# Kernel tuning notes

Hardware: AMD Instinct MI355X
Metric: run time of the kernel (lower is better)

## Reference

```python
import jax, jax.numpy as jnp
import numpy as np

N, E, F, HID, PC, HEADS = 100000, 1600000, 128, 128, 16, 4
RATIO = 0.8
NEG_SLOPE = 0.2
BIG_NEG = -1e9


def setup_inputs() -> dict:
    ks = jax.random.split(jax.random.key(0), 20)
    def g(k, shape, fan):
        return jax.random.normal(k, shape, jnp.float32) / np.float32(np.sqrt(fan))
    return {
        "x": jax.random.normal(ks[0], (N, F), jnp.float32),
        "edge_index": jax.random.randint(ks[1], (2, E), 0, N, dtype=jnp.int32),
        "edge_attr": jax.random.uniform(ks[2], (E, 1), dtype=jnp.float32),
        "W1": g(ks[3], (F, PC), F),
        "att_src1": g(ks[4], (HEADS, PC // HEADS), PC // HEADS),
        "att_dst1": g(ks[5], (HEADS, PC // HEADS), PC // HEADS),
        "We1": g(ks[6], (1, PC), 1),
        "att_edge1": g(ks[7], (HEADS, PC // HEADS), PC // HEADS),
        "b1": jnp.zeros((PC,), jnp.float32),
        "Wrel": g(ks[8], (PC, 1), PC),
        "brel": jnp.zeros((1,), jnp.float32),
        "Wroot": g(ks[9], (PC, 1), PC),
        "W2": g(ks[10], (PC, HID), PC),
        "att_src2": g(ks[11], (1, HID), HID),
        "att_dst2": g(ks[12], (1, HID), HID),
        "We2": g(ks[13], (1, HID), 1),
        "att_edge2": g(ks[14], (1, HID), HID),
        "b2": jnp.zeros((HID,), jnp.float32),
        "Wg": g(ks[15], (HID, 1), HID),
        "bg": jnp.zeros((1,), jnp.float32),
    }


def gat_conv(h_in, src, dst, e_attr, W, a_s, a_d, We, a_e, b, num_nodes, mask=None):
    """PyG GATConv (add_self_loops=False, eval-mode so dropout is identity)."""
    H, D = a_s.shape
    h = (h_in @ W).reshape(-1, H, D)                      # [N,H,D]
    al_s = jnp.einsum('nhd,hd->nh', h, a_s)               # alpha contribution of source
    al_d = jnp.einsum('nhd,hd->nh', h, a_d)               # alpha contribution of dest
    he = (e_attr @ We).reshape(-1, H, D)                  # [E,H,D] edge features
    al_e = jnp.einsum('ehd,hd->eh', he, a_e)              # [E,H]
    logits = jax.nn.leaky_relu(al_s[src] + al_d[dst] + al_e, NEG_SLOPE)  # [E,H]
    if mask is not None:
        logits = jnp.where(mask[:, None], logits, BIG_NEG)
    # segment softmax over incoming edges of each destination node
    m = jnp.maximum(jax.ops.segment_max(logits, dst, num_segments=num_nodes), BIG_NEG)
    num = jnp.exp(logits - m[dst])
    if mask is not None:
        num = jnp.where(mask[:, None], num, 0.0)
    den = jax.ops.segment_sum(num, dst, num_segments=num_nodes)
    coef = num / jnp.maximum(den[dst], 1e-16)             # [E,H]
    out = jax.ops.segment_sum(coef[:, :, None] * h[src], dst, num_segments=num_nodes)
    return out.reshape(num_nodes, H * D) + b


def _forward(x, edge_attr, W1, att_src1, att_dst1, We1, att_edge1, b1,
             Wrel, brel, Wroot, W2, att_src2, att_dst2, We2, att_edge2, b2,
             Wg, bg, edge_index):
    n = x.shape[0]
    src, dst = edge_index[0], edge_index[1]
    h1 = jax.nn.relu(gat_conv(x, src, dst, edge_attr, W1, att_src1, att_dst1, We1, att_edge1, b1, n))
    # --- SAGPooling: GraphConv score -> tanh -> top-k -> masked subgraph (n > node_threshold always) ---
    agg = jax.ops.segment_sum(h1[src], dst, num_segments=n)           # neighbor sum
    score = (agg @ Wrel + brel + h1 @ Wroot).reshape(-1)              # GraphConv(16 -> 1)
    k = int(np.ceil(RATIO * n))                                       # static
    vals, perm = jax.lax.top_k(score, k)
    new_idx = jnp.full((n,), -1, dtype=jnp.int32).at[perm].set(jnp.arange(k, dtype=jnp.int32))
    src_n, dst_n = new_idx[src], new_idx[dst]
    emask = (src_n >= 0) & (dst_n >= 0)                               # edges with both ends kept
    src2 = jnp.where(emask, src_n, 0)
    dst2 = jnp.where(emask, dst_n, 0)
    x2 = h1[perm] * jnp.tanh(vals)[:, None]                           # gate kept nodes
    h2 = jax.nn.relu(gat_conv(x2, src2, dst2, edge_attr, W2, att_src2, att_dst2, We2, att_edge2, b2, k, mask=emask))
    # --- AttentionalAggregation + MaxAggregation over the single graph (index = zeros) ---
    gate = jax.nn.softmax(h2 @ Wg + bg, axis=0)                       # [k,1]
    att = (gate * h2).sum(axis=0, keepdims=True)                      # [1,HID]
    mx = h2.max(axis=0, keepdims=True)                                # [1,HID]
    return jnp.concatenate([att, mx], axis=1)                         # [1,2*HID]


def reference(x, edge_index, edge_attr, W1, att_src1, att_dst1, We1, att_edge1, b1,
              Wrel, brel, Wroot, W2, att_src2, att_dst2, We2, att_edge2, b2, Wg, bg):
    return _forward(x, edge_attr, W1, att_src1, att_dst1, We1, att_edge1, b1,
                    Wrel, brel, Wroot, W2, att_src2, att_dst2, We2, att_edge2, b2,
                    Wg, bg, edge_index)
```

## Files before the change

### kernel.cpp

```cpp
#include <hip/hip_runtime.h>
#include <hip/hip_bf16.h>

#define Nn 100000
#define Ee 1600000
#define Kk 80000
#define NB ((Nn + 255) / 256)
#define NBK 196
#define CHK 8192
#define G2B 2048

typedef unsigned int uint;
typedef unsigned short ushort;

struct Scal {
    uint prefix, remaining, needEq;
    float c1[4];
    float c2;
    uint gmaxOrd;
    float deng;
    float attnum[128];
    uint mxOrd[128];
};

__device__ __forceinline__ uint f2ord(float f) {
    uint b = __float_as_uint(f);
    return (b & 0x80000000u) ? ~b : (b | 0x80000000u);
}
__device__ __forceinline__ float ord2f(uint u) {
    uint b = (u & 0x80000000u) ? (u ^ 0x80000000u) : ~u;
    return __uint_as_float(b);
}
__device__ __forceinline__ float lrelu(float v) { return v > 0.f ? v : 0.2f * v; }
__device__ __forceinline__ float2 bf2f2(uint u) {
    return make_float2(__uint_as_float(u << 16), __uint_as_float(u & 0xFFFF0000u));
}
__device__ __forceinline__ uint f2bf2(float a, float b) {
    __hip_bfloat162 h;
    h.x = __float2bfloat16(a);
    h.y = __float2bfloat16(b);
    return *(uint*)&h;
}

__global__ __launch_bounds__(256) void initK(uint* bcnt, uint* hist, Scal* sc) {
    int i = blockIdx.x * 256 + threadIdx.x;
    if (i < NBK) bcnt[i] = 0u;
    if (i < 256) hist[i] = 0u;
    if (i < 128) { sc->attnum[i] = 0.f; sc->mxOrd[i] = f2ord(0.0f); }
    if (i == 0) {
        sc->prefix = 0u; sc->remaining = Kk; sc->needEq = 0u;
        sc->deng = 0.f; sc->gmaxOrd = f2ord(-1e30f);
    }
}

__global__ void constK(const float* We1, const float* ae1, const float* We2, const float* ae2,
                       Scal* sc) {
    if (threadIdx.x == 0) {
        for (int h = 0; h < 4; h++) {
            float s = 0.f;
            for (int d = 0; d < 4; d++) s += We1[h * 4 + d] * ae1[h * 4 + d];
            sc->c1[h] = s;
        }
        float s2 = 0.f;
        for (int d = 0; d < 128; d++) s2 += We2[d] * ae2[d];
        sc->c2 = s2;
    }
}

__global__ __launch_bounds__(256) void nodeL1(const float* __restrict__ x,
                                              const float* __restrict__ W1,
                                              const float* __restrict__ as1,
                                              const float* __restrict__ ad1,
                                              float* __restrict__ hpre,
                                              float* __restrict__ alS1,
                                              float* __restrict__ alD1) {
    __shared__ float Ws[128 * 16];
    __shared__ float s_as[16], s_ad[16];
    for (int i = threadIdx.x; i < 2048; i += 256) Ws[i] = W1[i];
    if (threadIdx.x < 16) { s_as[threadIdx.x] = as1[threadIdx.x]; s_ad[threadIdx.x] = ad1[threadIdx.x]; }
    __syncthreads();
    int n = blockIdx.x * 256 + threadIdx.x;
    if (n >= Nn) return;
    float acc[16];
#pragma unroll
    for (int j = 0; j < 16; j++) acc[j] = 0.f;
    const float4* xr = (const float4*)(x + (size_t)n * 128);
    for (int t4 = 0; t4 < 32; t4++) {
        float4 xv = xr[t4];
#pragma unroll
        for (int j = 0; j < 16; j++) {
            acc[j] += xv.x * Ws[(t4 * 4 + 0) * 16 + j];
            acc[j] += xv.y * Ws[(t4 * 4 + 1) * 16 + j];
            acc[j] += xv.z * Ws[(t4 * 4 + 2) * 16 + j];
            acc[j] += xv.w * Ws[(t4 * 4 + 3) * 16 + j];
        }
    }
    float* hp = hpre + (size_t)n * 16;
#pragma unroll
    for (int j = 0; j < 16; j++) hp[j] = acc[j];
#pragma unroll
    for (int h = 0; h < 4; h++) {
        float s = 0.f, d = 0.f;
#pragma unroll
        for (int q = 0; q < 4; q++) {
            s += acc[h * 4 + q] * s_as[h * 4 + q];
            d += acc[h * 4 + q] * s_ad[h * 4 + q];
        }
        alS1[n * 4 + h] = s;
        alD1[n * 4 + h] = d;
    }
}

__global__ __launch_bounds__(256) void bucketCnt(const int* __restrict__ ei, uint* __restrict__ bcnt) {
    __shared__ uint h[NBK];
    if (threadIdx.x < NBK) h[threadIdx.x] = 0u;
    __syncthreads();
    for (int e = blockIdx.x * 256 + threadIdx.x; e < Ee; e += gridDim.x * 256)
        atomicAdd(&h[((uint)ei[Ee + e]) >> 9], 1u);
    __syncthreads();
    if (threadIdx.x < NBK && h[threadIdx.x]) atomicAdd(&bcnt[threadIdx.x], h[threadIdx.x]);
}

__global__ __launch_bounds__(256) void scanBk(const uint* __restrict__ bcnt, uint* __restrict__ boff,
                                              uint* __restrict__ gcur) {
    __shared__ uint s[256];
    int t = threadIdx.x;
    uint v = (t < NBK) ? bcnt[t] : 0u;
    s[t] = v;
    __syncthreads();
    for (int off = 1; off < 256; off <<= 1) {
        uint u = (t >= off) ? s[t - off] : 0u;
        __syncthreads();
        s[t] += u;
        __syncthreads();
    }
    if (t < NBK) { boff[t] = s[t] - v; gcur[t] = 0u; }
    if (t == 0) boff[NBK] = Ee;
}

__global__ __launch_bounds__(256) void binScat(const int* __restrict__ ei, const float* __restrict__ ea,
                                               const uint* __restrict__ boff, uint* __restrict__ gcur,
                                               uint2* __restrict__ bsE, ushort* __restrict__ bsD) {
    __shared__ uint h[NBK], base[NBK], h2[NBK];
    int t = threadIdx.x;
    if (t < NBK) h[t] = 0u;
    __syncthreads();
    int estart = blockIdx.x * CHK;
    int eend = min(Ee, estart + CHK);
    for (int e = estart + t; e < eend; e += 256)
        atomicAdd(&h[((uint)ei[Ee + e]) >> 9], 1u);
    __syncthreads();
    if (t < NBK) { base[t] = atomicAdd(&gcur[t], h[t]); h2[t] = 0u; }
    __syncthreads();
    for (int e = estart + t; e < eend; e += 256) {
        uint d = (uint)ei[Ee + e];
        uint b = d >> 9;
        uint r = atomicAdd(&h2[b], 1u);
        uint pos = boff[b] + base[b] + r;
        bsE[pos] = make_uint2((uint)ei[e], __float_as_uint(ea[e]));
        bsD[pos] = (ushort)(d & 511u);
    }
}

__global__ __launch_bounds__(256) void rankK(const uint* __restrict__ boff, const ushort* __restrict__ bsD,
                                             ushort* __restrict__ bsR, uint* __restrict__ deg) {
    __shared__ uint ldeg[512];
    int b = blockIdx.x, t = threadIdx.x;
    ldeg[t] = 0u; ldeg[t + 256] = 0u;
    __syncthreads();
    uint r0 = boff[b], r1 = boff[b + 1];
    for (uint i = r0 + t; i < r1; i += 256)
        bsR[i] = (ushort)atomicAdd(&ldeg[bsD[i]], 1u);
    __syncthreads();
    int nd = b * 512 + t;
    if (nd < Nn) deg[nd] = ldeg[t];
    nd = b * 512 + 256 + t;
    if (nd < Nn) deg[nd] = ldeg[256 + t];
}

__global__ __launch_bounds__(256) void scanA(const uint* __restrict__ deg, uint* __restrict__ rowstart,
                                             uint* __restrict__ blkSum) {
    __shared__ uint s[256];
    int i = blockIdx.x * 256 + threadIdx.x;
    uint v = (i < Nn) ? deg[i] : 0u;
    s[threadIdx.x] = v;
    __syncthreads();
    for (int off = 1; off < 256; off <<= 1) {
        uint t = (threadIdx.x >= off) ? s[threadIdx.x - off] : 0u;
        __syncthreads();
        s[threadIdx.x] += t;
        __syncthreads();
    }
    if (i < Nn) rowstart[i] = s[threadIdx.x] - v;
    if (threadIdx.x == 255) blkSum[blockIdx.x] = s[255];
}

__global__ __launch_bounds__(512) void scanB(const uint* __restrict__ blkSum, uint* __restrict__ blkOff) {
    __shared__ uint s[512];
    uint v = (threadIdx.x < NB) ? blkSum[threadIdx.x] : 0u;
    s[threadIdx.x] = v;
    __syncthreads();
    for (int off = 1; off < 512; off <<= 1) {
        uint t = (threadIdx.x >= off) ? s[threadIdx.x - off] : 0u;
        __syncthreads();
        s[threadIdx.x] += t;
        __syncthreads();
    }
    if (threadIdx.x < NB) blkOff[threadIdx.x] = s[threadIdx.x] - v;
}

__global__ __launch_bounds__(256) void scanC(uint* __restrict__ rowstart, const uint* __restrict__ blkOff) {
    int i = blockIdx.x * 256 + threadIdx.x;
    if (i < Nn) rowstart[i] += blkOff[blockIdx.x];
    if (i == 0) rowstart[Nn] = Ee;
}

__global__ __launch_bounds__(256) void placeK(const uint* __restrict__ boff, const uint2* __restrict__ bsE,
                                              const ushort* __restrict__ bsD, const ushort* __restrict__ bsR,
                                              const uint* __restrict__ rowstart, uint2* __restrict__ csr_p8) {
    __shared__ uint srs[512];
    int b = blockIdx.x, t = threadIdx.x;
    int nd = b * 512 + t;
    srs[t] = (nd < Nn) ? rowstart[nd] : 0u;
    nd = b * 512 + 256 + t;
    srs[256 + t] = (nd < Nn) ? rowstart[nd] : 0u;
    __syncthreads();
    uint r0 = boff[b], r1 = boff[b + 1];
    for (uint i = r0 + t; i < r1; i += 256)
        csr_p8[srs[bsD[i]] + bsR[i]] = bsE[i];
}

__global__ __launch_bounds__(256) void edgeP1(const uint2* __restrict__ csr_p8,
                                              const float* __restrict__ alS1,
                                              const Scal* __restrict__ scc,
                                              float4* __restrict__ csr_p1, int* __restrict__ csr_src) {
    int i = blockIdx.x * 256 + threadIdx.x;
    if (i >= Ee) return;
    uint2 p8 = csr_p8[i];
    int s = (int)p8.x;
    float eav = __uint_as_float(p8.y);
    float4 as = *(const float4*)(alS1 + (size_t)s * 4);
    float4 o;
    o.x = as.x + eav * scc->c1[0];
    o.y = as.y + eav * scc->c1[1];
    o.z = as.z + eav * scc->c1[2];
    o.w = as.w + eav * scc->c1[3];
    csr_p1[i] = o;
    csr_src[i] = s;
}

__global__ __launch_bounds__(256) void gather1e(const int* __restrict__ csr_src, const float* __restrict__ csr_p1,
                                                const uint* __restrict__ rowstart, const float* __restrict__ alD1,
                                                const float* __restrict__ hpre,
                                                const float* __restrict__ b1, const float* __restrict__ Wrel,
                                                const float* __restrict__ Wroot,
                                                float* __restrict__ h1, float* __restrict__ p,
                                                float* __restrict__ q) {
    int tid = blockIdx.x * 256 + threadIdx.x;
    if (tid >= Nn * 4) return;
    int d = tid >> 2, h = tid & 3;
    uint r0 = rowstart[d], r1 = rowstart[d + 1];
    float ad = alD1[tid];
    float den = 0.f;
    float4 acc = {0.f, 0.f, 0.f, 0.f};
#pragma unroll 8
    for (uint i = r0; i < r1; i++) {
        float e = __expf(lrelu(csr_p1[(size_t)i * 4 + h] + ad));
        float4 hv = *(const float4*)(hpre + (size_t)csr_src[i] * 16 + h * 4);
        den += e;
        acc.x += e * hv.x; acc.y += e * hv.y;
        acc.z += e * hv.z; acc.w += e * hv.w;
    }
    float inv = 1.f / fmaxf(den, 1e-16f);
    float4 o;
    o.x = fmaxf(acc.x * inv + b1[h * 4 + 0], 0.f);
    o.y = fmaxf(acc.y * inv + b1[h * 4 + 1], 0.f);
    o.z = fmaxf(acc.z * inv + b1[h * 4 + 2], 0.f);
    o.w = fmaxf(acc.w * inv + b1[h * 4 + 3], 0.f);
    *(float4*)(h1 + (size_t)d * 16 + h * 4) = o;
    float pp = o.x * Wrel[h * 4 + 0] + o.y * Wrel[h * 4 + 1] + o.z * Wrel[h * 4 + 2] + o.w * Wrel[h * 4 + 3];
    float qq = o.x * Wroot[h * 4 + 0] + o.y * Wroot[h * 4 + 1] + o.z * Wroot[h * 4 + 2] + o.w * Wroot[h * 4 + 3];
    pp += __shfl_xor(pp, 1); pp += __shfl_xor(pp, 2);
    qq += __shfl_xor(qq, 1); qq += __shfl_xor(qq, 2);
    if (h == 0) { p[d] = pp; q[d] = qq; }
}

__global__ __launch_bounds__(256) void scoreK2(const int* __restrict__ csr_src, const uint* __restrict__ rowstart,
                                               const float* __restrict__ p, const float* __restrict__ q,
                                               const float* __restrict__ brel,
                                               float* __restrict__ score, uint* __restrict__ dkey) {
    int d = blockIdx.x * 256 + threadIdx.x;
    if (d >= Nn) return;
    uint r0 = rowstart[d], r1 = rowstart[d + 1];
    float s = brel[0] + q[d];
#pragma unroll 8
    for (uint i = r0; i < r1; i++) s += p[csr_src[i]];
    score[d] = s;
    dkey[d] = ~f2ord(s);
}

__global__ __launch_bounds__(256) void histK(const uint* __restrict__ dkey, const Scal* __restrict__ sc,
                                             uint* __restrict__ hist, int shift) {
    __shared__ uint lh[256];
    lh[threadIdx.x] = 0u;
    __syncthreads();
    int i = blockIdx.x * 256 + threadIdx.x;
    if (i < Nn) {
        uint d = dkey[i];
        bool ok = (shift == 24) || ((d >> (shift + 8)) == sc->prefix);
        if (ok) atomicAdd(&lh[(d >> shift) & 255u], 1u);
    }
    __syncthreads();
    if (lh[threadIdx.x]) atomicAdd(&hist[threadIdx.x], lh[threadIdx.x]);
}

__global__ __launch_bounds__(256) void selP(Scal* sc, uint* hist) {
    __shared__ uint s[256];
    int t = threadIdx.x;
    uint c = hist[t];
    s[t] = c;
    __syncthreads();
    for (int off = 1; off < 256; off <<= 1) {
        uint v = (t >= off) ? s[t - off] : 0u;
        __syncthreads();
        s[t] += v;
        __syncthreads();
    }
    uint rem = sc->remaining;
    uint cum = s[t];
    uint cumex = cum - c;
    if (cum >= rem && cumex < rem) {
        sc->remaining = rem - cumex;
        sc->prefix = (sc->prefix << 8) | (uint)t;
    }
    hist[t] = 0u;
}

__global__ __launch_bounds__(256) void cntK(const uint* __restrict__ dkey, const Scal* __restrict__ sc,
                                            uint* __restrict__ blkLt, uint* __restrict__ blkEq) {
    int i = blockIdx.x * 256 + threadIdx.x;
    uint ut = sc->prefix;
    bool lt = (i < Nn) && (dkey[i] < ut);
    bool eq = (i < Nn) && (dkey[i] == ut);
    __shared__ uint sl[4], se[4];
    unsigned long long bl = __ballot(lt), be = __ballot(eq);
    int lane = threadIdx.x & 63, w = threadIdx.x >> 6;
    if (lane == 0) { sl[w] = (uint)__popcll(bl); se[w] = (uint)__popcll(be); }
    __syncthreads();
    if (threadIdx.x == 0) {
        blkLt[blockIdx.x] = sl[0] + sl[1] + sl[2] + sl[3];
        blkEq[blockIdx.x] = se[0] + se[1] + se[2] + se[3];
    }
}

__global__ __launch_bounds__(512) void prefP(Scal* sc, const uint* __restrict__ blkLt,
                                             const uint* __restrict__ blkEq, uint* __restrict__ eqPref) {
    __shared__ uint se[512];
    __shared__ uint sl[512];
    int t = threadIdx.x;
    uint e = (t < NB) ? blkEq[t] : 0u;
    uint l = (t < NB) ? blkLt[t] : 0u;
    se[t] = e; sl[t] = l;
    __syncthreads();
    for (int off = 1; off < 512; off <<= 1) {
        uint v1 = (t >= off) ? se[t - off] : 0u;
        uint v2 = (t >= off) ? sl[t - off] : 0u;
        __syncthreads();
        se[t] += v1; sl[t] += v2;
        __syncthreads();
    }
    if (t < NB) eqPref[t] = se[t] - e;
    if (t == 511) sc->needEq = Kk - sl[511];
}

__global__ __launch_bounds__(256) void keptK(const uint* __restrict__ dkey, const Scal* __restrict__ sc,
                                             const uint* __restrict__ eqPref, int* __restrict__ kept) {
    int i = blockIdx.x * 256 + threadIdx.x;
    uint ut = sc->prefix, needEq = sc->needEq;
    bool inr = i < Nn;
    uint d = inr ? dkey[i] : 0xFFFFFFFFu;
    bool isLt = inr && (d < ut);
    bool isEq = inr && (d == ut);
    __shared__ uint wcnt[4];
    unsigned long long mask = __ballot(isEq);
    int lane = threadIdx.x & 63, w = threadIdx.x >> 6;
    uint lanePre = (uint)__popcll(mask & ((1ull << lane) - 1ull));
    if (lane == 0) wcnt[w] = (uint)__popcll(mask);
    __syncthreads();
    uint wo = 0;
    for (int q = 0; q < 4; q++) if (q < w) wo += wcnt[q];
    uint rank = eqPref[blockIdx.x] + wo + lanePre;
    if (inr) kept[i] = (isLt || (isEq && rank < needEq)) ? 1 : 0;
}

__global__ __launch_bounds__(256) void nodeL2(const float* __restrict__ h1, const float* __restrict__ score,
                                              const int* __restrict__ kept, const float* __restrict__ W2,
                                              const float* __restrict__ as2, const float* __restrict__ ad2,
                                              __hip_bfloat162* __restrict__ h2b, float* __restrict__ alS2,
                                              float* __restrict__ alD2) {
    __shared__ float Ws[16 * 128];
    for (int i = threadIdx.x; i < 2048; i += 256) Ws[i] = W2[i];
    __syncthreads();
    int wid = (blockIdx.x * 256 + threadIdx.x) >> 6;
    int lane = threadIdx.x & 63;
    if (wid >= Nn) return;
    int n = wid;
    if (!kept[n]) return;
    float t = tanhf(score[n]);
    float x2[16];
    const float* hr = h1 + (size_t)n * 16;
#pragma unroll
    for (int j = 0; j < 16; j++) x2[j] = hr[j] * t;
    int d0 = 2 * lane, d1 = 2 * lane + 1;
    float a0 = 0.f, a1 = 0.f;
    const float2* Wv = (const float2*)Ws;
#pragma unroll
    for (int j = 0; j < 16; j++) {
        float2 wv = Wv[j * 64 + lane];
        a0 += x2[j] * wv.x;
        a1 += x2[j] * wv.y;
    }
    __hip_bfloat162 hb;
    hb.x = __float2bfloat16(a0);
    hb.y = __float2bfloat16(a1);
    h2b[(size_t)n * 64 + lane] = hb;
    float s = a0 * as2[d0] + a1 * as2[d1];
    float dd = a0 * ad2[d0] + a1 * ad2[d1];
#pragma unroll
    for (int off = 32; off; off >>= 1) { s += __shfl_xor(s, off); dd += __shfl_xor(dd, off); }
    if (lane == 0) { alS2[n] = s; alD2[n] = dd; }
}

__global__ __launch_bounds__(256) void edgeP2(const uint2* __restrict__ csr_p8, const int* __restrict__ kept,
                                              const float* __restrict__ alS2,
                                              const Scal* __restrict__ scc, float* __restrict__ csr_p2) {
    int i = blockIdx.x * 256 + threadIdx.x;
    if (i >= Ee) return;
    uint2 p8 = csr_p8[i];
    int s = (int)p8.x;
    float eav = __uint_as_float(p8.y);
    csr_p2[i] = kept[s] ? (alS2[s] + eav * scc->c2) : -1e30f;
}

__global__ __launch_bounds__(256) void gather2f(const int* __restrict__ csr_src,
                                                const float* __restrict__ csr_p2,
                                                const uint* __restrict__ rowstart, const int* __restrict__ kept,
                                                const float* __restrict__ alD2,
                                                const __hip_bfloat162* __restrict__ h2b, const float* __restrict__ b2,
                                                const float* __restrict__ Wg, const float* __restrict__ bg,
                                                float* __restrict__ pacc, float* __restrict__ pmx,
                                                float* __restrict__ pden) {
    __shared__ float sAtt[4][16][8];
    __shared__ float sMx[4][16][8];
    __shared__ float sDen[4];
    int w = threadIdx.x >> 6, lane = threadIdx.x & 63;
    int g = lane >> 4, t = lane & 15;
    float4 b2a = ((const float4*)b2)[t * 2], b2b = ((const float4*)b2)[t * 2 + 1];
    float4 wga = ((const float4*)Wg)[t * 2], wgb = ((const float4*)Wg)[t * 2 + 1];
    float bg0 = bg[0];
    const uint* h2u = (const uint*)h2b;
    float att[8], mx8[8], denP = 0.f;
#pragma unroll
    for (int j = 0; j < 8; j++) { att[j] = 0.f; mx8[j] = 0.f; }
    for (int n = blockIdx.x * 4 + w; n < Nn; n += G2B * 4) {
        if (!kept[n]) continue;
        float ad = alD2[n];
        uint r0 = rowstart[n];
        uint len = rowstart[n + 1] - r0;
        float den = 0.f;
        float acc[8];
#pragma unroll
        for (int d = 0; d < 8; d++) acc[d] = 0.f;
#pragma unroll 2
        for (uint base = 0; base < len; base += 4) {
            uint off = base + (uint)g;
            bool act = off < len;
            uint sidx = act ? (r0 + off) : (r0 + len - 1);
            float pv = act ? csr_p2[sidx] : -1e30f;
            float c = __expf(lrelu(pv + ad));
            int s = csr_src[sidx];
            uint4 hv = *(const uint4*)(h2u + (size_t)s * 64 + t * 4);
            den += c;
            float2 f;
            f = bf2f2(hv.x); acc[0] += c * f.x; acc[1] += c * f.y;
            f = bf2f2(hv.y); acc[2] += c * f.x; acc[3] += c * f.y;
            f = bf2f2(hv.z); acc[4] += c * f.x; acc[5] += c * f.y;
            f = bf2f2(hv.w); acc[6] += c * f.x; acc[7] += c * f.y;
        }
#pragma unroll
        for (int d = 0; d < 8; d++) {
            acc[d] += __shfl_xor(acc[d], 16);
            acc[d] += __shfl_xor(acc[d], 32);
        }
        den += __shfl_xor(den, 16);
        den += __shfl_xor(den, 32);
        float inv = 1.f / fmaxf(den, 1e-16f);
        float o[8];
        o[0] = fmaxf(acc[0] * inv + b2a.x, 0.f);
        o[1] = fmaxf(acc[1] * inv + b2a.y, 0.f);
        o[2] = fmaxf(acc[2] * inv + b2a.z, 0.f);
        o[3] = fmaxf(acc[3] * inv + b2a.w, 0.f);
        o[4] = fmaxf(acc[4] * inv + b2b.x, 0.f);
        o[5] = fmaxf(acc[5] * inv + b2b.y, 0.f);
        o[6] = fmaxf(acc[6] * inv + b2b.z, 0.f);
        o[7] = fmaxf(acc[7] * inv + b2b.w, 0.f);
        float gp = o[0] * wga.x + o[1] * wga.y + o[2] * wga.z + o[3] * wga.w +
                   o[4] * wgb.x + o[5] * wgb.y + o[6] * wgb.z + o[7] * wgb.w;
#pragma unroll
        for (int off = 8; off; off >>= 1) gp += __shfl_xor(gp, off);
        float e = __expf(gp + bg0);
        denP += e;
#pragma unroll
        for (int j = 0; j < 8; j++) {
            att[j] += e * o[j];
            mx8[j] = fmaxf(mx8[j], o[j]);
        }
    }
    if (g == 0) {
#pragma unroll
        for (int j = 0; j < 8; j++) { sAtt[w][t][j] = att[j]; sMx[w][t][j] = mx8[j]; }
    }
    if (lane == 0) sDen[w] = denP;
    __syncthreads();
    int tid = threadIdx.x;
    if (tid < 128) {
        int tt = tid >> 3, j = tid & 7;
        float a = sAtt[0][tt][j] + sAtt[1][tt][j] + sAtt[2][tt][j] + sAtt[3][tt][j];
        float m = fmaxf(fmaxf(sMx[0][tt][j], sMx[1][tt][j]), fmaxf(sMx[2][tt][j], sMx[3][tt][j]));
        pacc[(size_t)blockIdx.x * 128 + tid] = a;
        pmx[(size_t)blockIdx.x * 128 + tid] = m;
    }
    if (tid == 0) pden[blockIdx.x] = sDen[0] + sDen[1] + sDen[2] + sDen[3];
}

__global__ __launch_bounds__(256) void gateRed(const float* __restrict__ pacc, const float* __restrict__ pmx,
                                               const float* __restrict__ pden, Scal* sc) {
    __shared__ float r[256];
    int b = blockIdx.x, tid = threadIdx.x;
    if (b < 128) {
        float a = 0.f, m = 0.f;
        for (int i = tid; i < G2B; i += 256) {
            a += pacc[(size_t)i * 128 + b];
            m = fmaxf(m, pmx[(size_t)i * 128 + b]);
        }
        r[tid] = a;
        __syncthreads();
        for (int off = 128; off; off >>= 1) {
            if (tid < off) r[tid] += r[tid + off];
            __syncthreads();
        }
        float asum = r[0];
        __syncthreads();
        r[tid] = m;
        __syncthreads();
        for (int off = 128; off; off >>= 1) {
            if (tid < off) r[tid] = fmaxf(r[tid], r[tid + off]);
            __syncthreads();
        }
        if (tid == 0) { sc->attnum[b] = asum; sc->mxOrd[b] = f2ord(r[0]); }
    } else {
        float d = 0.f;
        for (int i = tid; i < G2B; i += 256) d += pden[i];
        r[tid] = d;
        __syncthreads();
        for (int off = 128; off; off >>= 1) {
            if (tid < off) r[tid] += r[tid + off];
            __syncthreads();
        }
        if (tid == 0) sc->deng = r[0];
    }
}

__global__ void outK(const Scal* sc, float* out) {
    int d = threadIdx.x;
    if (d < 128) {
        out[d] = sc->attnum[d] / sc->deng;
        out[128 + d] = ord2f(sc->mxOrd[d]);
    }
}

extern "C" void kernel_launch(void* const* d_in, const int* in_sizes, int n_in,
                              void* d_out, int out_size, void* d_ws, size_t ws_size,
                              hipStream_t stream) {
    const float* x = (const float*)d_in[0];
    const int* ei = (const int*)d_in[1];
    const float* ea = (const float*)d_in[2];
    const float* W1 = (const float*)d_in[3];
    const float* as1 = (const float*)d_in[4];
    const float* ad1 = (const float*)d_in[5];
    const float* We1 = (const float*)d_in[6];
    const float* ae1 = (const float*)d_in[7];
    const float* b1 = (const float*)d_in[8];
    const float* Wrel = (const float*)d_in[9];
    const float* brel = (const float*)d_in[10];
    const float* Wroot = (const float*)d_in[11];
    const float* W2 = (const float*)d_in[12];
    const float* as2 = (const float*)d_in[13];
    const float* ad2 = (const float*)d_in[14];
    const float* We2 = (const float*)d_in[15];
    const float* ae2 = (const float*)d_in[16];
    const float* b2 = (const float*)d_in[17];
    const float* Wg = (const float*)d_in[18];
    const float* bg = (const float*)d_in[19];
    float* out = (float*)d_out;

    float* base = (float*)d_ws;
    size_t o = 0;
    auto alloc = [&](size_t nf) { float* p2 = base + o; o += nf; return p2; };
    float4* csr_p1 = (float4*)alloc((size_t)Ee * 4);
    uint2* bsE = (uint2*)csr_p1;
    ushort* bsD = (ushort*)((float*)csr_p1 + (size_t)Ee * 2);
    ushort* bsR = (ushort*)((float*)csr_p1 + (size_t)Ee * 2 + Ee / 2);
    uint2* csr_p8 = (uint2*)alloc((size_t)Ee * 2);
    __hip_bfloat162* h2b = (__hip_bfloat162*)alloc((size_t)Nn * 64);
    float* hpre = alloc((size_t)Nn * 16);
    float* h1 = alloc((size_t)Nn * 16);
    int* csr_src = (int*)alloc(Ee);
    float* csr_p2 = alloc(Ee);
    float* pacc = alloc((size_t)G2B * 128);
    float* pmx = alloc((size_t)G2B * 128);
    float* pden = alloc(G2B);
    float* alS1 = alloc((size_t)Nn * 4);
    float* alD1 = alloc((size_t)Nn * 4);
    float* p = alloc(Nn);
    float* q = alloc(Nn);
    float* score = alloc(Nn);
    uint* dkey = (uint*)alloc(Nn);
    uint* deg = (uint*)alloc(Nn);
    int* kept = (int*)alloc(Nn);
    float* alS2 = alloc(Nn);
    float* alD2 = alloc(Nn);
    uint* rowstart = (uint*)alloc(Nn + 1);
    uint* hist = (uint*)alloc(256);
    uint* blkSum = (uint*)alloc(NB);
    uint* blkOff = (uint*)alloc(NB);
    uint* blkLt = (uint*)alloc(NB);
    uint* blkEq = (uint*)alloc(NB);
    uint* eqPref = (uint*)alloc(NB);
    uint* bcnt = (uint*)alloc(NBK);
    uint* boff = (uint*)alloc(NBK + 1);
    uint* gcur = (uint*)alloc(NBK);
    Scal* sc = (Scal*)alloc(512);

    auto cdiv = [](long a, long b) { return (int)((a + b - 1) / b); };

    initK<<<NB, 256, 0, stream>>>(bcnt, hist, sc);
    constK<<<1, 64, 0, stream>>>(We1, ae1, We2, ae2, sc);
    nodeL1<<<NB, 256, 0, stream>>>(x, W1, as1, ad1, hpre, alS1, alD1);
    bucketCnt<<<512, 256, 0, stream>>>(ei, bcnt);
    scanBk<<<1, 256, 0, stream>>>(bcnt, boff, gcur);
    binScat<<<cdiv(Ee, CHK), 256, 0, stream>>>(ei, ea, boff, gcur, bsE, bsD);
    rankK<<<NBK, 256, 0, stream>>>(boff, bsD, bsR, deg);
    scanA<<<NB, 256, 0, stream>>>(deg, rowstart, blkSum);
    scanB<<<1, 512, 0, stream>>>(blkSum, blkOff);
    scanC<<<NB, 256, 0, stream>>>(rowstart, blkOff);
    placeK<<<NBK, 256, 0, stream>>>(boff, bsE, bsD, bsR, rowstart, csr_p8);
    edgeP1<<<cdiv(Ee, 256), 256, 0, stream>>>(csr_p8, alS1, sc, csr_p1, csr_src);
    gather1e<<<cdiv((long)Nn * 4, 256), 256, 0, stream>>>(csr_src, (const float*)csr_p1, rowstart, alD1,
                                                          hpre, b1, Wrel, Wroot, h1, p, q);
    scoreK2<<<NB, 256, 0, stream>>>(csr_src, rowstart, p, q, brel, score, dkey);
    for (int shift = 24; shift >= 0; shift -= 8) {
        histK<<<NB, 256, 0, stream>>>(dkey, sc, hist, shift);
        selP<<<1, 256, 0, stream>>>(sc, hist);
    }
    cntK<<<NB, 256, 0, stream>>>(dkey, sc, blkLt, blkEq);
    prefP<<<1, 512, 0, stream>>>(sc, blkLt, blkEq, eqPref);
    keptK<<<NB, 256, 0, stream>>>(dkey, sc, eqPref, kept);
    nodeL2<<<cdiv(Nn, 4), 256, 0, stream>>>(h1, score, kept, W2, as2, ad2, h2b, alS2, alD2);
    edgeP2<<<cdiv(Ee, 256), 256, 0, stream>>>(csr_p8, kept, alS2, sc, csr_p2);
    gather2f<<<G2B, 256, 0, stream>>>(csr_src, csr_p2, rowstart, kept, alD2,
                                      h2b, b2, Wg, bg, pacc, pmx, pden);
    gateRed<<<129, 256, 0, stream>>>(pacc, pmx, pden, sc);
    outK<<<1, 128, 0, stream>>>(sc, out);
}
```

Before: 376.2 us.

## Fuse per-edge precompute kernels into gathers and fold constK into initK

Drops the edgeP1 and edgeP2 passes that built per-edge logit arrays (csr_p1, csr_p2, csr_src). The gather kernels now read the packed (src, edge_attr) CSR entry directly and compute the source logit plus edge term on the fly. For layer 2 this uses a per-node alS2k array that nodeL2 sets to -1e30 for dropped nodes. Constant computation is merged into initK, which saves launches and several full-edge write/read passes, at the cost of extra random gathers of alS1/alS2k inside the gather loops.

Result: faster. 342.5 us (-9.0%).

```diff
diff --git a/kernel.cpp b/kernel.cpp
--- a/kernel.cpp
+++ b/kernel.cpp
@@ -34,14 +34,10 @@
 __device__ __forceinline__ float2 bf2f2(uint u) {
     return make_float2(__uint_as_float(u << 16), __uint_as_float(u & 0xFFFF0000u));
 }
-__device__ __forceinline__ uint f2bf2(float a, float b) {
-    __hip_bfloat162 h;
-    h.x = __float2bfloat16(a);
-    h.y = __float2bfloat16(b);
-    return *(uint*)&h;
-}
-
-__global__ __launch_bounds__(256) void initK(uint* bcnt, uint* hist, Scal* sc) {
+
+__global__ __launch_bounds__(256) void initK(uint* bcnt, uint* hist, Scal* sc,
+                                             const float* We1, const float* ae1,
+                                             const float* We2, const float* ae2) {
     int i = blockIdx.x * 256 + threadIdx.x;
     if (i < NBK) bcnt[i] = 0u;
     if (i < 256) hist[i] = 0u;
@@ -49,12 +45,6 @@
     if (i == 0) {
         sc->prefix = 0u; sc->remaining = Kk; sc->needEq = 0u;
         sc->deng = 0.f; sc->gmaxOrd = f2ord(-1e30f);
-    }
-}
-
-__global__ void constK(const float* We1, const float* ae1, const float* We2, const float* ae2,
-                       Scal* sc) {
-    if (threadIdx.x == 0) {
         for (int h = 0; h < 4; h++) {
             float s = 0.f;
             for (int d = 0; d < 4; d++) s += We1[h * 4 + d] * ae1[h * 4 + d];
@@ -229,28 +219,10 @@
         csr_p8[srs[bsD[i]] + bsR[i]] = bsE[i];
 }
 
-__global__ __launch_bounds__(256) void edgeP1(const uint2* __restrict__ csr_p8,
-                                              const float* __restrict__ alS1,
-                                              const Scal* __restrict__ scc,
-                                              float4* __restrict__ csr_p1, int* __restrict__ csr_src) {
-    int i = blockIdx.x * 256 + threadIdx.x;
-    if (i >= Ee) return;
-    uint2 p8 = csr_p8[i];
-    int s = (int)p8.x;
-    float eav = __uint_as_float(p8.y);
-    float4 as = *(const float4*)(alS1 + (size_t)s * 4);
-    float4 o;
-    o.x = as.x + eav * scc->c1[0];
-    o.y = as.y + eav * scc->c1[1];
-    o.z = as.z + eav * scc->c1[2];
-    o.w = as.w + eav * scc->c1[3];
-    csr_p1[i] = o;
-    csr_src[i] = s;
-}
-
-__global__ __launch_bounds__(256) void gather1e(const int* __restrict__ csr_src, const float* __restrict__ csr_p1,
-                                                const uint* __restrict__ rowstart, const float* __restrict__ alD1,
-                                                const float* __restrict__ hpre,
+__global__ __launch_bounds__(256) void gather1f(const uint2* __restrict__ csr_p8,
+                                                const uint* __restrict__ rowstart,
+                                                const float* __restrict__ alS1, const float* __restrict__ alD1,
+                                                const float* __restrict__ hpre, const Scal* __restrict__ scc,
                                                 const float* __restrict__ b1, const float* __restrict__ Wrel,
                                                 const float* __restrict__ Wroot,
                                                 float* __restrict__ h1, float* __restrict__ p,
@@ -260,12 +232,15 @@
     int d = tid >> 2, h = tid & 3;
     uint r0 = rowstart[d], r1 = rowstart[d + 1];
     float ad = alD1[tid];
+    float c1h = scc->c1[h];
     float den = 0.f;
     float4 acc = {0.f, 0.f, 0.f, 0.f};
 #pragma unroll 8
     for (uint i = r0; i < r1; i++) {
-        float e = __expf(lrelu(csr_p1[(size_t)i * 4 + h] + ad));
-        float4 hv = *(const float4*)(hpre + (size_t)csr_src[i] * 16 + h * 4);
+        uint2 p8 = csr_p8[i];
+        int s = (int)p8.x;
+        float e = __expf(lrelu(alS1[s * 4 + h] + __uint_as_float(p8.y) * c1h + ad));
+        float4 hv = *(const float4*)(hpre + (size_t)s * 16 + h * 4);
         den += e;
         acc.x += e * hv.x; acc.y += e * hv.y;
         acc.z += e * hv.z; acc.w += e * hv.w;
@@ -284,7 +259,7 @@
     if (h == 0) { p[d] = pp; q[d] = qq; }
 }
 
-__global__ __launch_bounds__(256) void scoreK2(const int* __restrict__ csr_src, const uint* __restrict__ rowstart,
+__global__ __launch_bounds__(256) void scoreK2(const uint2* __restrict__ csr_p8, const uint* __restrict__ rowstart,
                                                const float* __restrict__ p, const float* __restrict__ q,
                                                const float* __restrict__ brel,
                                                float* __restrict__ score, uint* __restrict__ dkey) {
@@ -293,7 +268,7 @@
     uint r0 = rowstart[d], r1 = rowstart[d + 1];
     float s = brel[0] + q[d];
 #pragma unroll 8
-    for (uint i = r0; i < r1; i++) s += p[csr_src[i]];
+    for (uint i = r0; i < r1; i++) s += p[(int)csr_p8[i].x];
     score[d] = s;
     dkey[d] = ~f2ord(s);
 }
@@ -395,7 +370,7 @@
 __global__ __launch_bounds__(256) void nodeL2(const float* __restrict__ h1, const float* __restrict__ score,
                                               const int* __restrict__ kept, const float* __restrict__ W2,
                                               const float* __restrict__ as2, const float* __restrict__ ad2,
-                                              __hip_bfloat162* __restrict__ h2b, float* __restrict__ alS2,
+                                              __hip_bfloat162* __restrict__ h2b, float* __restrict__ alS2k,
                                               float* __restrict__ alD2) {
     __shared__ float Ws[16 * 128];
     for (int i = threadIdx.x; i < 2048; i += 256) Ws[i] = W2[i];
@@ -404,7 +379,7 @@
     int lane = threadIdx.x & 63;
     if (wid >= Nn) return;
     int n = wid;
-    if (!kept[n]) return;
+    if (!kept[n]) { if (lane == 0) alS2k[n] = -1e30f; return; }
     float t = tanhf(score[n]);
     float x2[16];
     const float* hr = h1 + (size_t)n * 16;
@@ -427,24 +402,13 @@
     float dd = a0 * ad2[d0] + a1 * ad2[d1];
 #pragma unroll
     for (int off = 32; off; off >>= 1) { s += __shfl_xor(s, off); dd += __shfl_xor(dd, off); }
-    if (lane == 0) { alS2[n] = s; alD2[n] = dd; }
-}
-
-__global__ __launch_bounds__(256) void edgeP2(const uint2* __restrict__ csr_p8, const int* __restrict__ kept,
-                                              const float* __restrict__ alS2,
-                                              const Scal* __restrict__ scc, float* __restrict__ csr_p2) {
-    int i = blockIdx.x * 256 + threadIdx.x;
-    if (i >= Ee) return;
-    uint2 p8 = csr_p8[i];
-    int s = (int)p8.x;
-    float eav = __uint_as_float(p8.y);
-    csr_p2[i] = kept[s] ? (alS2[s] + eav * scc->c2) : -1e30f;
-}
-
-__global__ __launch_bounds__(256) void gather2f(const int* __restrict__ csr_src,
-                                                const float* __restrict__ csr_p2,
+    if (lane == 0) { alS2k[n] = s; alD2[n] = dd; }
+}
+
+__global__ __launch_bounds__(256) void gather2g(const uint2* __restrict__ csr_p8,
                                                 const uint* __restrict__ rowstart, const int* __restrict__ kept,
-                                                const float* __restrict__ alD2,
+                                                const float* __restrict__ alS2k, const float* __restrict__ alD2,
+                                                const Scal* __restrict__ scc,
                                                 const __hip_bfloat162* __restrict__ h2b, const float* __restrict__ b2,
                                                 const float* __restrict__ Wg, const float* __restrict__ bg,
                                                 float* __restrict__ pacc, float* __restrict__ pmx,
@@ -457,6 +421,7 @@
     float4 b2a = ((const float4*)b2)[t * 2], b2b = ((const float4*)b2)[t * 2 + 1];
     float4 wga = ((const float4*)Wg)[t * 2], wgb = ((const float4*)Wg)[t * 2 + 1];
     float bg0 = bg[0];
+    float c2 = scc->c2;
     const uint* h2u = (const uint*)h2b;
     float att[8], mx8[8], denP = 0.f;
 #pragma unroll
@@ -475,9 +440,11 @@
             uint off = base + (uint)g;
             bool act = off < len;
             uint sidx = act ? (r0 + off) : (r0 + len - 1);
-            float pv = act ? csr_p2[sidx] : -1e30f;
+            uint2 p8 = csr_p8[sidx];
+            int s = (int)p8.x;
+            float pv = alS2k[s] + __uint_as_float(p8.y) * c2;
+            pv = act ? pv : -1e30f;
             float c = __expf(lrelu(pv + ad));
-            int s = csr_src[sidx];
             uint4 hv = *(const uint4*)(h2u + (size_t)s * 64 + t * 4);
             den += c;
             float2 f;
@@ -606,16 +573,13 @@
     float* base = (float*)d_ws;
     size_t o = 0;
     auto alloc = [&](size_t nf) { float* p2 = base + o; o += nf; return p2; };
-    float4* csr_p1 = (float4*)alloc((size_t)Ee * 4);
-    uint2* bsE = (uint2*)csr_p1;
-    ushort* bsD = (ushort*)((float*)csr_p1 + (size_t)Ee * 2);
-    ushort* bsR = (ushort*)((float*)csr_p1 + (size_t)Ee * 2 + Ee / 2);
+    uint2* bsE = (uint2*)alloc((size_t)Ee * 2);
+    ushort* bsD = (ushort*)alloc((size_t)Ee / 2);
+    ushort* bsR = (ushort*)alloc((size_t)Ee / 2);
     uint2* csr_p8 = (uint2*)alloc((size_t)Ee * 2);
     __hip_bfloat162* h2b = (__hip_bfloat162*)alloc((size_t)Nn * 64);
     float* hpre = alloc((size_t)Nn * 16);
     float* h1 = alloc((size_t)Nn * 16);
-    int* csr_src = (int*)alloc(Ee);
-    float* csr_p2 = alloc(Ee);
     float* pacc = alloc((size_t)G2B * 128);
     float* pmx = alloc((size_t)G2B * 128);
     float* pden = alloc(G2B);
@@ -627,7 +591,7 @@
     uint* dkey = (uint*)alloc(Nn);
     uint* deg = (uint*)alloc(Nn);
     int* kept = (int*)alloc(Nn);
-    float* alS2 = alloc(Nn);
+    float* alS2k = alloc(Nn);
     float* alD2 = alloc(Nn);
     uint* rowstart = (uint*)alloc(Nn + 1);
     uint* hist = (uint*)alloc(256);
@@ -643,8 +607,7 @@
 
     auto cdiv = [](long a, long b) { return (int)((a + b - 1) / b); };
 
-    initK<<<NB, 256, 0, stream>>>(bcnt, hist, sc);
-    constK<<<1, 64, 0, stream>>>(We1, ae1, We2, ae2, sc);
+    initK<<<NB, 256, 0, stream>>>(bcnt, hist, sc, We1, ae1, We2, ae2);
     nodeL1<<<NB, 256, 0, stream>>>(x, W1, as1, ad1, hpre, alS1, alD1);
     bucketCnt<<<512, 256, 0, stream>>>(ei, bcnt);
     scanBk<<<1, 256, 0, stream>>>(bcnt, boff, gcur);
@@ -654,10 +617,9 @@
     scanB<<<1, 512, 0, stream>>>(blkSum, blkOff);
     scanC<<<NB, 256, 0, stream>>>(rowstart, blkOff);
     placeK<<<NBK, 256, 0, stream>>>(boff, bsE, bsD, bsR, rowstart, csr_p8);
-    edgeP1<<<cdiv(Ee, 256), 256, 0, stream>>>(csr_p8, alS1, sc, csr_p1, csr_src);
-    gather1e<<<cdiv((long)Nn * 4, 256), 256, 0, stream>>>(csr_src, (const float*)csr_p1, rowstart, alD1,
-                                                          hpre, b1, Wrel, Wroot, h1, p, q);
-    scoreK2<<<NB, 256, 0, stream>>>(csr_src, rowstart, p, q, brel, score, dkey);
+    gather1f<<<cdiv((long)Nn * 4, 256), 256, 0, stream>>>(csr_p8, rowstart, alS1, alD1, hpre, sc,
+                                                          b1, Wrel, Wroot, h1, p, q);
+    scoreK2<<<NB, 256, 0, stream>>>(csr_p8, rowstart, p, q, brel, score, dkey);
     for (int shift = 24; shift >= 0; shift -= 8) {
         histK<<<NB, 256, 0, stream>>>(dkey, sc, hist, shift);
         selP<<<1, 256, 0, stream>>>(sc, hist);
@@ -665,9 +627,8 @@
     cntK<<<NB, 256, 0, stream>>>(dkey, sc, blkLt, blkEq);
     prefP<<<1, 512, 0, stream>>>(sc, blkLt, blkEq, eqPref);
     keptK<<<NB, 256, 0, stream>>>(dkey, sc, eqPref, kept);
-    nodeL2<<<cdiv(Nn, 4), 256, 0, stream>>>(h1, score, kept, W2, as2, ad2, h2b, alS2, alD2);
-    edgeP2<<<cdiv(Ee, 256), 256, 0, stream>>>(csr_p8, kept, alS2, sc, csr_p2);
-    gather2f<<<G2B, 256, 0, stream>>>(csr_src, csr_p2, rowstart, kept, alD2,
+    nodeL2<<<cdiv(Nn, 4), 256, 0, stream>>>(h1, score, kept, W2, as2, ad2, h2b, alS2k, alD2);
+    gather2g<<<G2B, 256, 0, stream>>>(csr_p8, rowstart, kept, alS2k, alD2, sc,
                                       h2b, b2, Wg, bg, pacc, pmx, pden);
     gateRed<<<129, 256, 0, stream>>>(pacc, pmx, pden, sc);
     outK<<<1, 128, 0, stream>>>(sc, out);
```
